# Kernel optimization log

Measured on AMD Instinct MI355X. Metric: run time of the kernel, lower is better.

The kernel has to match this reference:

```python
import jax, jax.numpy as jnp
import numpy as np

N_PTS = 1_000_000
N_CORNERS = 2_000_000  # per-level corner count (table has +1 zero row for misses)
FEAT_DIM = 16
MAX_LEVEL = 12
FEAT_LEVELS = 3  # levels MAX_LEVEL, MAX_LEVEL-1, MAX_LEVEL-2
POLY_INT = True


def setup_inputs() -> dict:
    key = jax.random.key(0)
    ks = jax.random.split(key, 8)
    x = jax.random.uniform(ks[0], (N_PTS, 3), jnp.float32, -1.0, 1.0)
    std = 0.05
    feats = [std * jax.random.normal(ks[1 + i], (N_CORNERS + 1, FEAT_DIM), jnp.float32)
             for i in range(FEAT_LEVELS)]
    # last row is the zero feature for unobserved nodes
    feats = [f.at[-1].set(0.0) for f in feats]
    idxs = [jax.random.randint(ks[4 + i], (N_PTS, 8), 0, N_CORNERS, dtype=jnp.int64)
            for i in range(FEAT_LEVELS)]
    return {"x": x,
            "feat0": feats[0], "feat1": feats[1], "feat2": feats[2],
            "idx0": idxs[0], "idx1": idxs[1], "idx2": idxs[2]}


def _interp_coeffs(x, level, polynomial_on=POLY_INT):
    # coords = 2^level * (x*0.5 + 0.5); d = frac(coords)
    coords = (2.0 ** level) * (x * 0.5 + 0.5)
    d = coords - jnp.floor(coords)                      # [N,3]
    t = 3.0 * d**2 - 2.0 * d**3 if polynomial_on else d
    tx, ty, tz = t[:, 0], t[:, 1], t[:, 2]
    ux, uy, uz = 1.0 - tx, 1.0 - ty, 1.0 - tz
    # corner order matches torch.stack((p0..p7)): z fastest, then y, then x
    p = jnp.stack([ux * uy * uz, ux * uy * tz, ux * ty * uz, ux * ty * tz,
                   tx * uy * uz, tx * uy * tz, tx * ty * uz, tx * ty * tz],
                  axis=1)                               # [N,8]
    return p


def reference(x, feat0, feat1, feat2, idx0, idx1, idx2):
    feats = (feat0, feat1, feat2)
    idxs = (idx0, idx1, idx2)
    out = jnp.zeros((x.shape[0], FEAT_DIM), dtype=x.dtype)
    for i in range(FEAT_LEVELS):
        level = MAX_LEVEL - i
        p = _interp_coeffs(x, level)                    # [N,8]
        g = feats[i][idxs[i]]                           # [N,8,D] gather
        out = out + jnp.einsum("nk,nkd->nd", p, g)
    return out
```

## Files before the change

kernel.cpp:

```cpp
#include <hip/hip_runtime.h>


typedef float v4f __attribute__((ext_vector_type(4)));
typedef int   v4i __attribute__((ext_vector_type(4)));

__device__ __forceinline__ void accum_level(
    long long pt, int sub, float cx, float cy, float cz,
    const v4f* __restrict__ feat, const int* __restrict__ idx,
    v4f& acc)
{
    float dx = cx - floorf(cx);
    float dy = cy - floorf(cy);
    float dz = cz - floorf(cz);
    float tx = dx * dx * (3.0f - 2.0f * dx);
    float ty = dy * dy * (3.0f - 2.0f * dy);
    float tz = dz * dz * (3.0f - 2.0f * dz);
    float ux = 1.0f - tx, uy = 1.0f - ty, uz = 1.0f - tz;

    float p[8];
    p[0] = ux * uy * uz;
    p[1] = ux * uy * tz;
    p[2] = ux * ty * uz;
    p[3] = ux * ty * tz;
    p[4] = tx * uy * uz;
    p[5] = tx * uy * tz;
    p[6] = tx * ty * uz;
    p[7] = tx * ty * tz;

    const v4i* iv = (const v4i*)(idx + pt * 8);
    v4i ia = __builtin_nontemporal_load(iv);
    v4i ib = __builtin_nontemporal_load(iv + 1);
    int id[8] = { ia.x, ia.y, ia.z, ia.w, ib.x, ib.y, ib.z, ib.w };

#pragma unroll
    for (int k = 0; k < 8; ++k) {
        v4f g = feat[(long long)id[k] * 4 + sub];
        acc.x = fmaf(p[k], g.x, acc.x);
        acc.y = fmaf(p[k], g.y, acc.y);
        acc.z = fmaf(p[k], g.z, acc.z);
        acc.w = fmaf(p[k], g.w, acc.w);
    }
}

__global__ __launch_bounds__(256) void FeatureOctree_74749610820348_kernel(
    const float* __restrict__ x,
    const v4f* __restrict__ f0,
    const v4f* __restrict__ f1,
    const v4f* __restrict__ f2,
    const int* __restrict__ i0,
    const int* __restrict__ i1,
    const int* __restrict__ i2,
    v4f* __restrict__ out,
    int n_pts)
{
    long long tid = (long long)blockIdx.x * blockDim.x + threadIdx.x;
    long long pt = tid >> 2;
    int sub = (int)(tid & 3);
    if (pt >= n_pts) return;

    float xv = __builtin_nontemporal_load(x + pt * 3 + 0);
    float yv = __builtin_nontemporal_load(x + pt * 3 + 1);
    float zv = __builtin_nontemporal_load(x + pt * 3 + 2);

    float bx = xv * 0.5f + 0.5f;
    float by = yv * 0.5f + 0.5f;
    float bz = zv * 0.5f + 0.5f;

    v4f acc = (v4f){0.0f, 0.0f, 0.0f, 0.0f};

    accum_level(pt, sub, 4096.0f * bx, 4096.0f * by, 4096.0f * bz, f0, i0, acc);
    accum_level(pt, sub, 2048.0f * bx, 2048.0f * by, 2048.0f * bz, f1, i1, acc);
    accum_level(pt, sub, 1024.0f * bx, 1024.0f * by, 1024.0f * bz, f2, i2, acc);

    __builtin_nontemporal_store(acc, out + pt * 4 + sub);
}

extern "C" void kernel_launch(void* const* d_in, const int* in_sizes, int n_in,
                              void* d_out, int out_size, void* d_ws, size_t ws_size,
                              hipStream_t stream) {
    const float* x  = (const float*)d_in[0];
    const v4f*   f0 = (const v4f*)d_in[1];
    const v4f*   f1 = (const v4f*)d_in[2];
    const v4f*   f2 = (const v4f*)d_in[3];
    const int*   i0 = (const int*)d_in[4];
    const int*   i1 = (const int*)d_in[5];
    const int*   i2 = (const int*)d_in[6];
    v4f* out = (v4f*)d_out;

    int n_pts = in_sizes[0] / 3;
    long long total = (long long)n_pts * 4;
    int block = 256;
    int grid = (int)((total + block - 1) / block);

    FeatureOctree_74749610820348_kernel<<<grid, block, 0, stream>>>(
        x, f0, f1, f2, i0, i1, i2, out, n_pts);
}
```

Before: 787.0 us.

## Partition gathers into index-range phases with block sync for cache locality

Each thread now handles two points and all 16 features per point instead of four threads per point. The feature gathers are split into about eight phases by high bits of the row index, with a __syncthreads between phases, so that blocks tend to touch the same slice of each feature table at once and get more L2/MALL hits. The cost is a much larger register footprint (48 indices plus 8 accumulators per thread), a divergent per-corner branch in every phase, eight passes of coefficient recomputation, and lower thread-level parallelism for hiding gather latency. Phase alignment is only enforced within a block, so blocks across the GPU can drift out of step.

```diff
diff --git a/kernel.cpp b/kernel.cpp
--- a/kernel.cpp
+++ b/kernel.cpp
@@ -4,45 +4,15 @@
 typedef float v4f __attribute__((ext_vector_type(4)));
 typedef int   v4i __attribute__((ext_vector_type(4)));
 
-__device__ __forceinline__ void accum_level(
-    long long pt, int sub, float cx, float cy, float cz,
-    const v4f* __restrict__ feat, const int* __restrict__ idx,
-    v4f& acc)
-{
-    float dx = cx - floorf(cx);
-    float dy = cy - floorf(cy);
-    float dz = cz - floorf(cz);
-    float tx = dx * dx * (3.0f - 2.0f * dx);
-    float ty = dy * dy * (3.0f - 2.0f * dy);
-    float tz = dz * dz * (3.0f - 2.0f * dz);
-    float ux = 1.0f - tx, uy = 1.0f - ty, uz = 1.0f - tz;
+#define ACC_FMA(A, PK, G)                      \
+    do {                                       \
+        (A).x = fmaf((PK), (G).x, (A).x);      \
+        (A).y = fmaf((PK), (G).y, (A).y);      \
+        (A).z = fmaf((PK), (G).z, (A).z);      \
+        (A).w = fmaf((PK), (G).w, (A).w);      \
+    } while (0)
 
-    float p[8];
-    p[0] = ux * uy * uz;
-    p[1] = ux * uy * tz;
-    p[2] = ux * ty * uz;
-    p[3] = ux * ty * tz;
-    p[4] = tx * uy * uz;
-    p[5] = tx * uy * tz;
-    p[6] = tx * ty * uz;
-    p[7] = tx * ty * tz;
-
-    const v4i* iv = (const v4i*)(idx + pt * 8);
-    v4i ia = __builtin_nontemporal_load(iv);
-    v4i ib = __builtin_nontemporal_load(iv + 1);
-    int id[8] = { ia.x, ia.y, ia.z, ia.w, ib.x, ib.y, ib.z, ib.w };
-
-#pragma unroll
-    for (int k = 0; k < 8; ++k) {
-        v4f g = feat[(long long)id[k] * 4 + sub];
-        acc.x = fmaf(p[k], g.x, acc.x);
-        acc.y = fmaf(p[k], g.y, acc.y);
-        acc.z = fmaf(p[k], g.z, acc.z);
-        acc.w = fmaf(p[k], g.w, acc.w);
-    }
-}
-
-__global__ __launch_bounds__(256) void FeatureOctree_74749610820348_kernel(
+__global__ __launch_bounds__(256, 4) void FeatureOctree_74749610820348_kernel(
     const float* __restrict__ x,
     const v4f* __restrict__ f0,
     const v4f* __restrict__ f1,
@@ -51,28 +21,105 @@
     const int* __restrict__ i1,
     const int* __restrict__ i2,
     v4f* __restrict__ out,
-    int n_pts)
+    int n_pts, int shift, int nphase)
 {
     long long tid = (long long)blockIdx.x * blockDim.x + threadIdx.x;
-    long long pt = tid >> 2;
-    int sub = (int)(tid & 3);
-    if (pt >= n_pts) return;
+    long long pt0 = tid * 2;
 
-    float xv = __builtin_nontemporal_load(x + pt * 3 + 0);
-    float yv = __builtin_nontemporal_load(x + pt * 3 + 1);
-    float zv = __builtin_nontemporal_load(x + pt * 3 + 2);
+    bool valid0 = (pt0     < n_pts);
+    bool valid1 = (pt0 + 1 < n_pts);
 
-    float bx = xv * 0.5f + 0.5f;
-    float by = yv * 0.5f + 0.5f;
-    float bz = zv * 0.5f + 0.5f;
+    int id[2][3][8];
+    const int* __restrict__ itab[3] = { i0, i1, i2 };
+#pragma unroll
+    for (int w = 0; w < 2; ++w) {
+        bool v = w ? valid1 : valid0;
+#pragma unroll
+        for (int lv = 0; lv < 3; ++lv) {
+            if (v) {
+                const v4i* iv = (const v4i*)(itab[lv] + (pt0 + w) * 8);
+                v4i ia = __builtin_nontemporal_load(iv);
+                v4i ib = __builtin_nontemporal_load(iv + 1);
+                id[w][lv][0] = ia.x; id[w][lv][1] = ia.y;
+                id[w][lv][2] = ia.z; id[w][lv][3] = ia.w;
+                id[w][lv][4] = ib.x; id[w][lv][5] = ib.y;
+                id[w][lv][6] = ib.z; id[w][lv][7] = ib.w;
+            } else {
+#pragma unroll
+                for (int k = 0; k < 8; ++k) id[w][lv][k] = -1;
+            }
+        }
+    }
 
-    v4f acc = (v4f){0.0f, 0.0f, 0.0f, 0.0f};
+    float bx[2], by[2], bz[2];
+#pragma unroll
+    for (int w = 0; w < 2; ++w) {
+        bool v = w ? valid1 : valid0;
+        float xv = 0.f, yv = 0.f, zv = 0.f;
+        if (v) {
+            xv = __builtin_nontemporal_load(x + (pt0 + w) * 3 + 0);
+            yv = __builtin_nontemporal_load(x + (pt0 + w) * 3 + 1);
+            zv = __builtin_nontemporal_load(x + (pt0 + w) * 3 + 2);
+        }
+        bx[w] = xv * 0.5f + 0.5f;
+        by[w] = yv * 0.5f + 0.5f;
+        bz[w] = zv * 0.5f + 0.5f;
+    }
 
-    accum_level(pt, sub, 4096.0f * bx, 4096.0f * by, 4096.0f * bz, f0, i0, acc);
-    accum_level(pt, sub, 2048.0f * bx, 2048.0f * by, 2048.0f * bz, f1, i1, acc);
-    accum_level(pt, sub, 1024.0f * bx, 1024.0f * by, 1024.0f * bz, f2, i2, acc);
+    v4f acc[2][4];
+#pragma unroll
+    for (int w = 0; w < 2; ++w)
+#pragma unroll
+        for (int q = 0; q < 4; ++q) acc[w][q] = (v4f){0.f, 0.f, 0.f, 0.f};
 
-    __builtin_nontemporal_store(acc, out + pt * 4 + sub);
+    const v4f* __restrict__ ftab[3] = { f0, f1, f2 };
+
+    for (int h = 0; h < nphase; ++h) {
+#pragma unroll
+        for (int w = 0; w < 2; ++w) {
+#pragma unroll
+            for (int lv = 0; lv < 3; ++lv) {
+                const float scl = (lv == 0) ? 4096.0f : (lv == 1) ? 2048.0f : 1024.0f;
+                float cx = scl * bx[w], cy = scl * by[w], cz = scl * bz[w];
+                float dx = cx - floorf(cx);
+                float dy = cy - floorf(cy);
+                float dz = cz - floorf(cz);
+                float tx = dx * dx * (3.0f - 2.0f * dx);
+                float ty = dy * dy * (3.0f - 2.0f * dy);
+                float tz = dz * dz * (3.0f - 2.0f * dz);
+                float ux = 1.0f - tx, uy = 1.0f - ty, uz = 1.0f - tz;
+#pragma unroll
+                for (int k = 0; k < 8; ++k) {
+                    int idk = id[w][lv][k];
+                    if ((idk >> shift) == h) {
+                        float pk = ((k & 4) ? tx : ux)
+                                 * ((k & 2) ? ty : uy)
+                                 * ((k & 1) ? tz : uz);
+                        const v4f* row = ftab[lv] + (long long)idk * 4;
+                        v4f g0 = row[0];
+                        v4f g1 = row[1];
+                        v4f g2 = row[2];
+                        v4f g3 = row[3];
+                        ACC_FMA(acc[w][0], pk, g0);
+                        ACC_FMA(acc[w][1], pk, g1);
+                        ACC_FMA(acc[w][2], pk, g2);
+                        ACC_FMA(acc[w][3], pk, g3);
+                    }
+                }
+            }
+        }
+        __syncthreads();
+    }
+
+#pragma unroll
+    for (int w = 0; w < 2; ++w) {
+        bool v = w ? valid1 : valid0;
+        if (v) {
+#pragma unroll
+            for (int q = 0; q < 4; ++q)
+                __builtin_nontemporal_store(acc[w][q], out + (pt0 + w) * 4 + q);
+        }
+    }
 }
 
 extern "C" void kernel_launch(void* const* d_in, const int* in_sizes, int n_in,
@@ -88,10 +135,16 @@
     v4f* out = (v4f*)d_out;
 
     int n_pts = in_sizes[0] / 3;
-    long long total = (long long)n_pts * 4;
+
+    long long rows = (long long)in_sizes[1] / 16;
+    int shift = 0;
+    while (((rows - 1) >> shift) >= 8) ++shift;
+    int nphase = (int)(((rows - 1) >> shift) + 1);
+
+    long long threads = (n_pts + 1) / 2;
     int block = 256;
-    int grid = (int)((total + block - 1) / block);
+    int grid = (int)((threads + block - 1) / block);
 
     FeatureOctree_74749610820348_kernel<<<grid, block, 0, stream>>>(
-        x, f0, f1, f2, i0, i1, i2, out, n_pts);
+        x, f0, f1, f2, i0, i1, i2, out, n_pts, shift, nphase);
 }
```

New measurement: 2.098 ms. 167% more time.
